# Optimization experiments

Measured on AMD Instinct MI355X. Metric: run time of the kernel, lower is better.

The kernel has to match this reference:

```python
import jax, jax.numpy as jnp
import numpy as np

B, T, U, E, DIN = 32, 512, 1024, 1024, 256

def setup_inputs() -> dict:
    key = jax.random.key(0)
    ks = jax.random.split(key, 12)
    s = lambda d: 1.0 / np.sqrt(d)
    bias = jnp.zeros((4 * U,), jnp.float32).at[U:2 * U].set(2.0)  # forget-gate bias init = 2
    return {
        'inputs': jax.random.normal(ks[0], (B, DIN), jnp.float32),
        'h': jax.random.normal(ks[1], (B, U), jnp.float32) * 0.1,
        'c': jax.random.normal(ks[2], (B, U), jnp.float32) * 0.1,
        'speech_encode': jax.random.normal(ks[3], (B, T, E), jnp.float32),
        'encodestate': jax.random.normal(ks[4], (B, T, U), jnp.float32),
        'Wa_w': jax.random.normal(ks[5], (U, U), jnp.float32) * s(U),
        'Wa_b': jnp.zeros((U,), jnp.float32),
        'va_w': jax.random.normal(ks[6], (U, 1), jnp.float32) * s(U),
        'va_b': jnp.zeros((1,), jnp.float32),
        'kernel': jax.random.normal(ks[7], (DIN + E, 4 * U), jnp.float32) * s(DIN + E),
        'rec_kernel': jax.random.normal(ks[8], (U, 4 * U), jnp.float32) * s(U),
        'bias': bias,
    }


def reference(inputs, h, c, speech_encode, encodestate, Wa_w, Wa_b, va_w, va_b, kernel, rec_kernel, bias):
    # Bahdanau attention: score = va(tanh(Wa(h)[:,None,:] + encodestate))
    query = h @ Wa_w + Wa_b                                   # [B,U]
    scores = jnp.tanh(query[:, None, :] + encodestate) @ va_w  # [B,T,1]
    logits = jnp.squeeze(scores + va_b, axis=2)                # [B,T]
    attn = jax.nn.softmax(logits, axis=-1)                     # [B,T]
    context = jnp.einsum('bt,bte->be', attn, speech_encode)    # [B,E]
    # LSTM cell step on [inputs; context]
    x = jnp.concatenate([inputs, context], axis=1)             # [B,DIN+E]
    z = x @ kernel + h @ rec_kernel + bias                     # [B,4U]
    zi, zf, zg, zo = jnp.split(z, 4, axis=1)
    c_new = jax.nn.sigmoid(zf) * c + jax.nn.sigmoid(zi) * jnp.tanh(zg)
    h_new = jax.nn.sigmoid(zo) * jnp.tanh(c_new)
    return (h_new, h_new, c_new)  # (lstmout, [h, c])
```

## Files before the change

kernel.cpp:

```cpp
#include <hip/hip_runtime.h>
#include <hip/hip_bf16.h>

#define B 32
#define T 512
#define U 1024
#define E 1024
#define DIN 256
#define N4 4096

__device__ __forceinline__ float fast_tanh(float x) {
    float e = __expf(2.0f * x);
    return 1.0f - 2.0f / (e + 1.0f);
}
__device__ __forceinline__ float fast_sigmoid(float x) {
    return 1.0f / (1.0f + __expf(-x));
}

__global__ __launch_bounds__(256) void k1_qpart(const float* __restrict__ h,
                                                const float* __restrict__ Wa_w,
                                                float* __restrict__ qpart) {
    const int uc = blockIdx.x;
    const int kc = blockIdx.y;
    const int tid = threadIdx.x;
    const int k0 = kc * 64;
    __shared__ float hs[32][64];
    #pragma unroll
    for (int i = 0; i < 8; ++i) {
        int flat = i * 256 + tid;
        int b = flat >> 6, kk = flat & 63;
        hs[b][kk] = h[b * U + k0 + kk];
    }
    __syncthreads();
    const int jg = tid & 63;
    const int b0 = (tid >> 6) * 8;
    const int j = uc * 256 + jg * 4;
    float4 acc[8];
    #pragma unroll
    for (int p = 0; p < 8; ++p) acc[p] = make_float4(0.f, 0.f, 0.f, 0.f);
    const float* Wp = Wa_w + (size_t)k0 * U + j;
    #pragma unroll 4
    for (int kk = 0; kk < 64; ++kk) {
        float4 w = *(const float4*)(Wp + (size_t)kk * U);
        #pragma unroll
        for (int p = 0; p < 8; ++p) {
            float xv = hs[b0 + p][kk];
            acc[p].x += xv * w.x; acc[p].y += xv * w.y;
            acc[p].z += xv * w.z; acc[p].w += xv * w.w;
        }
    }
    #pragma unroll
    for (int p = 0; p < 8; ++p)
        *(float4*)(qpart + ((size_t)(kc * 32 + b0 + p)) * U + j) = acc[p];
}

__global__ __launch_bounds__(256) void k1b_qreduce(const float* __restrict__ qpart,
                                                   const float* __restrict__ Wa_b,
                                                   float* __restrict__ query) {
    int idx = blockIdx.x * 256 + threadIdx.x;
    int b = idx >> 10, u = idx & 1023;
    float s = Wa_b[u];
    #pragma unroll
    for (int kc = 0; kc < 16; ++kc) s += qpart[((size_t)(kc * 32 + b)) * U + u];
    query[idx] = s;
}

__global__ __launch_bounds__(256) void k2_logits(const float* __restrict__ query,
                                                 const float* __restrict__ enc,
                                                 const float* __restrict__ va_w,
                                                 const float* __restrict__ va_b,
                                                 float* __restrict__ logits) {
    int gw = blockIdx.x * 4 + (threadIdx.x >> 6);
    int lane = threadIdx.x & 63;
    int b = gw >> 9, t = gw & 511;
    const float4* e4 = (const float4*)(enc + ((size_t)(b * T + t)) * U);
    const float4* q4 = (const float4*)(query + (size_t)b * U);
    const float4* v4 = (const float4*)va_w;
    float acc = 0.f;
    #pragma unroll
    for (int i = 0; i < 4; ++i) {
        int idx = i * 64 + lane;
        float4 e = e4[idx], q = q4[idx], v = v4[idx];
        acc += fast_tanh(e.x + q.x) * v.x;
        acc += fast_tanh(e.y + q.y) * v.y;
        acc += fast_tanh(e.z + q.z) * v.z;
        acc += fast_tanh(e.w + q.w) * v.w;
    }
    #pragma unroll
    for (int off = 32; off > 0; off >>= 1) acc += __shfl_xor(acc, off);
    if (lane == 0) logits[b * T + t] = acc + va_b[0];
}

__global__ __launch_bounds__(256) void k3_softmax(const float* __restrict__ logits,
                                                  float* __restrict__ attn) {
    int b = blockIdx.x, tid = threadIdx.x, lane = tid & 63, w = tid >> 6;
    float l0 = logits[b * T + tid], l1 = logits[b * T + 256 + tid];
    float m = fmaxf(l0, l1);
    #pragma unroll
    for (int off = 32; off > 0; off >>= 1) m = fmaxf(m, __shfl_xor(m, off));
    __shared__ float sm[4], ss[4];
    if (lane == 0) sm[w] = m;
    __syncthreads();
    float M = fmaxf(fmaxf(sm[0], sm[1]), fmaxf(sm[2], sm[3]));
    float e0 = __expf(l0 - M), e1 = __expf(l1 - M);
    float s = e0 + e1;
    #pragma unroll
    for (int off = 32; off > 0; off >>= 1) s += __shfl_xor(s, off);
    if (lane == 0) ss[w] = s;
    __syncthreads();
    float inv = 1.0f / (ss[0] + ss[1] + ss[2] + ss[3]);
    attn[b * T + tid] = e0 * inv;
    attn[b * T + 256 + tid] = e1 * inv;
}

__global__ __launch_bounds__(256) void k4_ctxpart(const float* __restrict__ attn,
                                                  const float* __restrict__ speech,
                                                  float* __restrict__ ctxpart) {
    int bid = blockIdx.x;
    int tc = bid & 7, ec = (bid >> 3) & 3, b = bid >> 5;
    int e = ec * 256 + threadIdx.x;
    int t0 = tc * 64;
    const float* sp = speech + ((size_t)(b * T + t0)) * E + e;
    const float* at = attn + b * T + t0;
    float acc = 0.f;
    #pragma unroll 4
    for (int tt = 0; tt < 64; ++tt) acc += at[tt] * sp[(size_t)tt * E];
    ctxpart[((size_t)(tc * 32 + b)) * E + e] = acc;
}

__global__ __launch_bounds__(256) void k4b_ctxreduce(const float* __restrict__ ctxpart,
                                                     float* __restrict__ context) {
    int idx = blockIdx.x * 256 + threadIdx.x;
    int b = idx >> 10, e = idx & 1023;
    float s = 0.f;
    #pragma unroll
    for (int tc = 0; tc < 8; ++tc) s += ctxpart[((size_t)(tc * 32 + b)) * E + e];
    context[idx] = s;
}

__global__ __launch_bounds__(256) void k5_zpart(const float* __restrict__ xin,
                                                const float* __restrict__ ctx,
                                                const float* __restrict__ h,
                                                const float* __restrict__ Wk,
                                                const float* __restrict__ Wr,
                                                float* __restrict__ zpart) {
    const int jc = blockIdx.x;
    const int kc = blockIdx.y;
    const int tid = threadIdx.x;
    const int k0 = kc * 128;
    __shared__ float xs[32][128];
    #pragma unroll
    for (int i = 0; i < 16; ++i) {
        int flat = i * 256 + tid;
        int b = flat >> 7, kk = flat & 127;
        int k = k0 + kk;
        float v;
        if (k < DIN)          v = xin[b * DIN + k];
        else if (k < DIN + E) v = ctx[b * E + (k - DIN)];
        else                  v = h[b * U + (k - DIN - E)];
        xs[b][kk] = v;
    }
    __syncthreads();
    const int jg = tid & 63;
    const int b0 = (tid >> 6) * 8;
    const int j = jc * 256 + jg * 4;
    const float* Wrow = (k0 < DIN + E) ? (Wk + (size_t)k0 * N4 + j)
                                       : (Wr + (size_t)(k0 - (DIN + E)) * N4 + j);
    float4 acc[8];
    #pragma unroll
    for (int p = 0; p < 8; ++p) acc[p] = make_float4(0.f, 0.f, 0.f, 0.f);
    #pragma unroll 4
    for (int kk = 0; kk < 128; ++kk) {
        float4 w = *(const float4*)(Wrow + (size_t)kk * N4);
        #pragma unroll
        for (int p = 0; p < 8; ++p) {
            float xv = xs[b0 + p][kk];
            acc[p].x += xv * w.x; acc[p].y += xv * w.y;
            acc[p].z += xv * w.z; acc[p].w += xv * w.w;
        }
    }
    #pragma unroll
    for (int p = 0; p < 8; ++p)
        *(float4*)(zpart + ((size_t)(kc * 32 + b0 + p)) * N4 + j) = acc[p];
}

__global__ __launch_bounds__(256) void k6_gates(const float* __restrict__ zpart,
                                                const float* __restrict__ bias,
                                                const float* __restrict__ c,
                                                float* __restrict__ out) {
    int idx = blockIdx.x * 256 + threadIdx.x;
    int b = idx >> 10, u = idx & 1023;
    float zi = bias[u], zf = bias[U + u], zg = bias[2 * U + u], zo = bias[3 * U + u];
    for (int kc = 0; kc < 18; ++kc) {
        const float* zp = zpart + ((size_t)(kc * 32 + b)) * N4;
        zi += zp[u]; zf += zp[U + u]; zg += zp[2 * U + u]; zo += zp[3 * U + u];
    }
    float cn = fast_sigmoid(zf) * c[idx] + fast_sigmoid(zi) * fast_tanh(zg);
    float hn = fast_sigmoid(zo) * fast_tanh(cn);
    out[idx] = hn;
    out[32768 + idx] = hn;
    out[65536 + idx] = cn;
}

extern "C" void kernel_launch(void* const* d_in, const int* in_sizes, int n_in,
                              void* d_out, int out_size, void* d_ws, size_t ws_size,
                              hipStream_t stream) {
    const float* inputs = (const float*)d_in[0];
    const float* h      = (const float*)d_in[1];
    const float* c      = (const float*)d_in[2];
    const float* speech = (const float*)d_in[3];
    const float* enc    = (const float*)d_in[4];
    const float* Wa_w   = (const float*)d_in[5];
    const float* Wa_b   = (const float*)d_in[6];
    const float* va_w   = (const float*)d_in[7];
    const float* va_b   = (const float*)d_in[8];
    const float* Wk     = (const float*)d_in[9];
    const float* Wr     = (const float*)d_in[10];
    const float* bias   = (const float*)d_in[11];
    float* out = (float*)d_out;
    float* ws  = (float*)d_ws;

    float* query   = ws;
    float* qpart   = ws + 32768;
    float* logits  = ws + 557056;
    float* attn    = ws + 573440;
    float* ctxpart = ws + 589824;
    float* context = ws + 851968;
    float* zpart   = ws + 884736;

    k1_qpart<<<dim3(4, 16), 256, 0, stream>>>(h, Wa_w, qpart);
    k1b_qreduce<<<128, 256, 0, stream>>>(qpart, Wa_b, query);
    k2_logits<<<4096, 256, 0, stream>>>(query, enc, va_w, va_b, logits);
    k3_softmax<<<32, 256, 0, stream>>>(logits, attn);
    k4_ctxpart<<<1024, 256, 0, stream>>>(attn, speech, ctxpart);
    k4b_ctxreduce<<<128, 256, 0, stream>>>(ctxpart, context);
    k5_zpart<<<dim3(16, 18), 256, 0, stream>>>(inputs, context, h, Wk, Wr, zpart);
    k6_gates<<<128, 256, 0, stream>>>(zpart, bias, c, out);
}
```

Measured before the change: 269.5 us.

## Replace split-K partial buffers and reduce kernels with atomic accumulation

The separate reduce kernels for query, context and gate pre-activations are removed. Partial results are now added directly with atomicAdd into buffers pre-seeded with biases or zeros by a new init kernel. Split-K GEMM blocks are retiled into smaller output tiles so more blocks run in parallel, and weight and speech loads are batched eight at a time to raise memory-level parallelism. This cuts launch count and partial-buffer traffic, at the cost of many float atomics and results that are no longer bit-deterministic.

```diff
diff --git a/kernel.cpp b/kernel.cpp
--- a/kernel.cpp
+++ b/kernel.cpp
@@ -16,52 +16,64 @@
     return 1.0f / (1.0f + __expf(-x));
 }
 
-__global__ __launch_bounds__(256) void k1_qpart(const float* __restrict__ h,
+__global__ __launch_bounds__(256) void k0_init(const float* __restrict__ Wa_b,
+                                               const float* __restrict__ bias,
+                                               float* __restrict__ query,
+                                               float* __restrict__ zacc,
+                                               float* __restrict__ ctx) {
+    int idx = blockIdx.x * 256 + threadIdx.x;
+    if (idx < 32768) {
+        query[idx] = Wa_b[idx & 1023];
+    } else if (idx < 163840) {
+        int z = idx - 32768;
+        zacc[z] = bias[z & 4095];
+    } else {
+        ctx[idx - 163840] = 0.f;
+    }
+}
+
+__global__ __launch_bounds__(256) void k1_query(const float* __restrict__ h,
                                                 const float* __restrict__ Wa_w,
-                                                float* __restrict__ qpart) {
-    const int uc = blockIdx.x;
+                                                float* __restrict__ query) {
+    const int jc = blockIdx.x;
     const int kc = blockIdx.y;
     const int tid = threadIdx.x;
-    const int k0 = kc * 64;
-    __shared__ float hs[32][64];
-    #pragma unroll
-    for (int i = 0; i < 8; ++i) {
-        int flat = i * 256 + tid;
-        int b = flat >> 6, kk = flat & 63;
-        hs[b][kk] = h[b * U + k0 + kk];
-    }
-    __syncthreads();
-    const int jg = tid & 63;
-    const int b0 = (tid >> 6) * 8;
-    const int j = uc * 256 + jg * 4;
-    float4 acc[8];
-    #pragma unroll
-    for (int p = 0; p < 8; ++p) acc[p] = make_float4(0.f, 0.f, 0.f, 0.f);
-    const float* Wp = Wa_w + (size_t)k0 * U + j;
-    #pragma unroll 4
-    for (int kk = 0; kk < 64; ++kk) {
-        float4 w = *(const float4*)(Wp + (size_t)kk * U);
-        #pragma unroll
-        for (int p = 0; p < 8; ++p) {
-            float xv = hs[b0 + p][kk];
-            acc[p].x += xv * w.x; acc[p].y += xv * w.y;
-            acc[p].z += xv * w.z; acc[p].w += xv * w.w;
+    const int k0 = kc * 32;
+    __shared__ float hs[32][32];
+    {
+        int flat = tid * 4;
+        int b = flat >> 5, kk = flat & 31;
+        *(float4*)&hs[b][kk] = *(const float4*)&h[b * U + k0 + kk];
+    }
+    __syncthreads();
+    const int jg = tid & 31;
+    const int b0 = (tid >> 5) * 4;
+    const int j = jc * 128 + jg * 4;
+    const float4* Wp = (const float4*)(Wa_w + (size_t)k0 * U + j);
+    float4 acc[4];
+    #pragma unroll
+    for (int p = 0; p < 4; ++p) acc[p] = make_float4(0.f, 0.f, 0.f, 0.f);
+    #pragma unroll 1
+    for (int kk = 0; kk < 32; kk += 8) {
+        float4 w[8];
+        #pragma unroll
+        for (int u = 0; u < 8; ++u) w[u] = Wp[(size_t)(kk + u) * (U / 4)];
+        #pragma unroll
+        for (int u = 0; u < 8; ++u) {
+            #pragma unroll
+            for (int p = 0; p < 4; ++p) {
+                float xv = hs[b0 + p][kk + u];
+                acc[p].x += xv * w[u].x; acc[p].y += xv * w[u].y;
+                acc[p].z += xv * w[u].z; acc[p].w += xv * w[u].w;
+            }
         }
     }
     #pragma unroll
-    for (int p = 0; p < 8; ++p)
-        *(float4*)(qpart + ((size_t)(kc * 32 + b0 + p)) * U + j) = acc[p];
-}
-
-__global__ __launch_bounds__(256) void k1b_qreduce(const float* __restrict__ qpart,
-                                                   const float* __restrict__ Wa_b,
-                                                   float* __restrict__ query) {
-    int idx = blockIdx.x * 256 + threadIdx.x;
-    int b = idx >> 10, u = idx & 1023;
-    float s = Wa_b[u];
-    #pragma unroll
-    for (int kc = 0; kc < 16; ++kc) s += qpart[((size_t)(kc * 32 + b)) * U + u];
-    query[idx] = s;
+    for (int p = 0; p < 4; ++p) {
+        float* q = query + (size_t)(b0 + p) * U + j;
+        atomicAdd(q + 0, acc[p].x); atomicAdd(q + 1, acc[p].y);
+        atomicAdd(q + 2, acc[p].z); atomicAdd(q + 3, acc[p].w);
+    }
 }
 
 __global__ __launch_bounds__(256) void k2_logits(const float* __restrict__ query,
@@ -75,15 +87,19 @@
     const float4* e4 = (const float4*)(enc + ((size_t)(b * T + t)) * U);
     const float4* q4 = (const float4*)(query + (size_t)b * U);
     const float4* v4 = (const float4*)va_w;
-    float acc = 0.f;
+    float4 e[4], q[4], v[4];
     #pragma unroll
     for (int i = 0; i < 4; ++i) {
         int idx = i * 64 + lane;
-        float4 e = e4[idx], q = q4[idx], v = v4[idx];
-        acc += fast_tanh(e.x + q.x) * v.x;
-        acc += fast_tanh(e.y + q.y) * v.y;
-        acc += fast_tanh(e.z + q.z) * v.z;
-        acc += fast_tanh(e.w + q.w) * v.w;
+        e[i] = e4[idx]; q[i] = q4[idx]; v[i] = v4[idx];
+    }
+    float acc = 0.f;
+    #pragma unroll
+    for (int i = 0; i < 4; ++i) {
+        acc += fast_tanh(e[i].x + q[i].x) * v[i].x;
+        acc += fast_tanh(e[i].y + q[i].y) * v[i].y;
+        acc += fast_tanh(e[i].z + q[i].z) * v[i].z;
+        acc += fast_tanh(e[i].w + q[i].w) * v[i].w;
     }
     #pragma unroll
     for (int off = 32; off > 0; off >>= 1) acc += __shfl_xor(acc, off);
@@ -112,88 +128,97 @@
     attn[b * T + 256 + tid] = e1 * inv;
 }
 
-__global__ __launch_bounds__(256) void k4_ctxpart(const float* __restrict__ attn,
-                                                  const float* __restrict__ speech,
-                                                  float* __restrict__ ctxpart) {
+__global__ __launch_bounds__(256) void k4_ctx(const float* __restrict__ attn,
+                                              const float* __restrict__ speech,
+                                              float* __restrict__ ctx) {
     int bid = blockIdx.x;
-    int tc = bid & 7, ec = (bid >> 3) & 3, b = bid >> 5;
-    int e = ec * 256 + threadIdx.x;
-    int t0 = tc * 64;
-    const float* sp = speech + ((size_t)(b * T + t0)) * E + e;
-    const float* at = attn + b * T + t0;
-    float acc = 0.f;
-    #pragma unroll 4
-    for (int tt = 0; tt < 64; ++tt) acc += at[tt] * sp[(size_t)tt * E];
-    ctxpart[((size_t)(tc * 32 + b)) * E + e] = acc;
-}
-
-__global__ __launch_bounds__(256) void k4b_ctxreduce(const float* __restrict__ ctxpart,
-                                                     float* __restrict__ context) {
-    int idx = blockIdx.x * 256 + threadIdx.x;
-    int b = idx >> 10, e = idx & 1023;
-    float s = 0.f;
-    #pragma unroll
-    for (int tc = 0; tc < 8; ++tc) s += ctxpart[((size_t)(tc * 32 + b)) * E + e];
-    context[idx] = s;
-}
-
-__global__ __launch_bounds__(256) void k5_zpart(const float* __restrict__ xin,
-                                                const float* __restrict__ ctx,
-                                                const float* __restrict__ h,
-                                                const float* __restrict__ Wk,
-                                                const float* __restrict__ Wr,
-                                                float* __restrict__ zpart) {
+    int tc = bid & 15, b = bid >> 4;
+    int t0 = tc * 32;
+    __shared__ float sat[32];
+    if (threadIdx.x < 32) sat[threadIdx.x] = attn[b * T + t0 + threadIdx.x];
+    __syncthreads();
+    int e = threadIdx.x * 4;
+    const float4* sp = (const float4*)(speech + ((size_t)(b * T + t0)) * E + e);
+    float4 acc = make_float4(0.f, 0.f, 0.f, 0.f);
+    #pragma unroll 1
+    for (int tt = 0; tt < 32; tt += 8) {
+        float4 s[8];
+        #pragma unroll
+        for (int u = 0; u < 8; ++u) s[u] = sp[(size_t)(tt + u) * (E / 4)];
+        #pragma unroll
+        for (int u = 0; u < 8; ++u) {
+            float a = sat[tt + u];
+            acc.x += a * s[u].x; acc.y += a * s[u].y;
+            acc.z += a * s[u].z; acc.w += a * s[u].w;
+        }
+    }
+    float* cp = ctx + (size_t)b * E + e;
+    atomicAdd(cp + 0, acc.x); atomicAdd(cp + 1, acc.y);
+    atomicAdd(cp + 2, acc.z); atomicAdd(cp + 3, acc.w);
+}
+
+__global__ __launch_bounds__(256) void k5_z(const float* __restrict__ xin,
+                                            const float* __restrict__ ctx,
+                                            const float* __restrict__ h,
+                                            const float* __restrict__ Wk,
+                                            const float* __restrict__ Wr,
+                                            float* __restrict__ zacc) {
     const int jc = blockIdx.x;
     const int kc = blockIdx.y;
     const int tid = threadIdx.x;
     const int k0 = kc * 128;
     __shared__ float xs[32][128];
     #pragma unroll
-    for (int i = 0; i < 16; ++i) {
-        int flat = i * 256 + tid;
+    for (int i = 0; i < 4; ++i) {
+        int flat = (i * 256 + tid) * 4;
         int b = flat >> 7, kk = flat & 127;
         int k = k0 + kk;
-        float v;
-        if (k < DIN)          v = xin[b * DIN + k];
-        else if (k < DIN + E) v = ctx[b * E + (k - DIN)];
-        else                  v = h[b * U + (k - DIN - E)];
-        xs[b][kk] = v;
-    }
-    __syncthreads();
-    const int jg = tid & 63;
-    const int b0 = (tid >> 6) * 8;
-    const int j = jc * 256 + jg * 4;
-    const float* Wrow = (k0 < DIN + E) ? (Wk + (size_t)k0 * N4 + j)
-                                       : (Wr + (size_t)(k0 - (DIN + E)) * N4 + j);
-    float4 acc[8];
-    #pragma unroll
-    for (int p = 0; p < 8; ++p) acc[p] = make_float4(0.f, 0.f, 0.f, 0.f);
-    #pragma unroll 4
-    for (int kk = 0; kk < 128; ++kk) {
-        float4 w = *(const float4*)(Wrow + (size_t)kk * N4);
-        #pragma unroll
-        for (int p = 0; p < 8; ++p) {
-            float xv = xs[b0 + p][kk];
-            acc[p].x += xv * w.x; acc[p].y += xv * w.y;
-            acc[p].z += xv * w.z; acc[p].w += xv * w.w;
+        float4 v;
+        if (k < DIN)          v = *(const float4*)&xin[b * DIN + k];
+        else if (k < DIN + E) v = *(const float4*)&ctx[b * E + (k - DIN)];
+        else                  v = *(const float4*)&h[b * U + (k - DIN - E)];
+        *(float4*)&xs[b][kk] = v;
+    }
+    __syncthreads();
+    const int jg = tid & 31;
+    const int b0 = (tid >> 5) * 4;
+    const int j = jc * 128 + jg * 4;
+    const float* Wbase = (k0 < DIN + E) ? (Wk + (size_t)k0 * N4)
+                                        : (Wr + (size_t)(k0 - DIN - E) * N4);
+    const float4* Wp = (const float4*)(Wbase + j);
+    float4 acc[4];
+    #pragma unroll
+    for (int p = 0; p < 4; ++p) acc[p] = make_float4(0.f, 0.f, 0.f, 0.f);
+    #pragma unroll 1
+    for (int kk = 0; kk < 128; kk += 8) {
+        float4 w[8];
+        #pragma unroll
+        for (int u = 0; u < 8; ++u) w[u] = Wp[(size_t)(kk + u) * (N4 / 4)];
+        #pragma unroll
+        for (int u = 0; u < 8; ++u) {
+            #pragma unroll
+            for (int p = 0; p < 4; ++p) {
+                float xv = xs[b0 + p][kk + u];
+                acc[p].x += xv * w[u].x; acc[p].y += xv * w[u].y;
+                acc[p].z += xv * w[u].z; acc[p].w += xv * w[u].w;
+            }
         }
     }
     #pragma unroll
-    for (int p = 0; p < 8; ++p)
-        *(float4*)(zpart + ((size_t)(kc * 32 + b0 + p)) * N4 + j) = acc[p];
-}
-
-__global__ __launch_bounds__(256) void k6_gates(const float* __restrict__ zpart,
-                                                const float* __restrict__ bias,
+    for (int p = 0; p < 4; ++p) {
+        float* zp = zacc + (size_t)(b0 + p) * N4 + j;
+        atomicAdd(zp + 0, acc[p].x); atomicAdd(zp + 1, acc[p].y);
+        atomicAdd(zp + 2, acc[p].z); atomicAdd(zp + 3, acc[p].w);
+    }
+}
+
+__global__ __launch_bounds__(256) void k6_gates(const float* __restrict__ zacc,
                                                 const float* __restrict__ c,
                                                 float* __restrict__ out) {
     int idx = blockIdx.x * 256 + threadIdx.x;
     int b = idx >> 10, u = idx & 1023;
-    float zi = bias[u], zf = bias[U + u], zg = bias[2 * U + u], zo = bias[3 * U + u];
-    for (int kc = 0; kc < 18; ++kc) {
-        const float* zp = zpart + ((size_t)(kc * 32 + b)) * N4;
-        zi += zp[u]; zf += zp[U + u]; zg += zp[2 * U + u]; zo += zp[3 * U + u];
-    }
+    const float* zb = zacc + (size_t)b * N4;
+    float zi = zb[u], zf = zb[U + u], zg = zb[2 * U + u], zo = zb[3 * U + u];
     float cn = fast_sigmoid(zf) * c[idx] + fast_sigmoid(zi) * fast_tanh(zg);
     float hn = fast_sigmoid(zo) * fast_tanh(cn);
     out[idx] = hn;
@@ -219,20 +244,17 @@
     float* out = (float*)d_out;
     float* ws  = (float*)d_ws;
 
-    float* query   = ws;
-    float* qpart   = ws + 32768;
-    float* logits  = ws + 557056;
-    float* attn    = ws + 573440;
-    float* ctxpart = ws + 589824;
-    float* context = ws + 851968;
-    float* zpart   = ws + 884736;
-
-    k1_qpart<<<dim3(4, 16), 256, 0, stream>>>(h, Wa_w, qpart);
-    k1b_qreduce<<<128, 256, 0, stream>>>(qpart, Wa_b, query);
+    float* query  = ws;
+    float* zacc   = ws + 32768;
+    float* ctx    = ws + 163840;
+    float* logits = ws + 196608;
+    float* attn   = ws + 212992;
+
+    k0_init<<<768, 256, 0, stream>>>(Wa_b, bias, query, zacc, ctx);
+    k1_query<<<dim3(8, 32), 256, 0, stream>>>(h, Wa_w, query);
     k2_logits<<<4096, 256, 0, stream>>>(query, enc, va_w, va_b, logits);
     k3_softmax<<<32, 256, 0, stream>>>(logits, attn);
-    k4_ctxpart<<<1024, 256, 0, stream>>>(attn, speech, ctxpart);
-    k4b_ctxreduce<<<128, 256, 0, stream>>>(ctxpart, context);
-    k5_zpart<<<dim3(16, 18), 256, 0, stream>>>(inputs, context, h, Wk, Wr, zpart);
-    k6_gates<<<128, 256, 0, stream>>>(zpart, bias, c, out);
-}
+    k4_ctx<<<512, 256, 0, stream>>>(attn, speech, ctx);
+    k5_z<<<dim3(32, 18), 256, 0, stream>>>(inputs, ctx, h, Wk, Wr, zacc);
+    k6_gates<<<128, 256, 0, stream>>>(zacc, c, out);
+}
```

Measured after the change: 282.6 us. 1.05x slower.
